# Kernel tuning notes

Measured on AMD Instinct MI355X. Metric: run time of the kernel, lower is better.

Reference implementation:

```python
import jax, jax.numpy as jnp
import numpy as np

RCR = 5.2          # radial cutoff
RCA = 3.5          # angular cutoff
ETA_R = 16.0
SHF_R = jnp.asarray(0.9 + 0.26875 * np.arange(16), jnp.float32)          # 16 radial shifts
ZETA = 32.0
SHF_Z = jnp.asarray((2 * np.arange(8) + 1) * np.pi / 16.0, jnp.float32)  # 8 angle shifts
ETA_A = 8.0
SHF_A = jnp.asarray(0.9 + 0.65 * np.arange(4), jnp.float32)              # 4 angular radial shifts
NUM_SPECIES = 4
NUM_PAIRS = NUM_SPECIES * (NUM_SPECIES + 1) // 2  # 10


def _pair_index_table():
    idx = np.zeros((NUM_SPECIES, NUM_SPECIES), np.int32)
    c = 0
    for s1 in range(NUM_SPECIES):
        for s2 in range(s1, NUM_SPECIES):
            idx[s1, s2] = c
            idx[s2, s1] = c
            c += 1
    return jnp.asarray(idx)

PAIR_IDX = _pair_index_table()


def _cutoff(d, rc):
    return jnp.where(d <= rc, 0.5 * jnp.cos(jnp.pi * d / rc) + 0.5, 0.0)


def setup_inputs() -> dict:
    key = jax.random.key(0)
    k1, k2 = jax.random.split(key)
    species = jax.random.randint(k1, (32, 48), 0, NUM_SPECIES, dtype=jnp.int32)
    coords = jax.random.uniform(k2, (32, 48, 3), jnp.float32) * 7.0  # 7 Angstrom box
    return {"species": species, "coords": coords}


def reference(species, coords):
    B, A = species.shape
    dt = coords.dtype
    # vec[b,i,j] = coords[j] - coords[i]
    diff = coords[:, None, :, :] - coords[:, :, None, :]           # [B,A,A,3]
    d2 = jnp.sum(diff * diff, -1)
    eye = jnp.eye(A, dtype=bool)
    dist = jnp.sqrt(jnp.where(eye, 1.0, d2))                        # safe on diagonal
    valid = (species[:, :, None] >= 0) & (species[:, None, :] >= 0) & (~eye)

    # ---------- radial AEV ----------
    fc_r = jnp.where(valid & (dist <= RCR), _cutoff(dist, RCR), 0.0)
    rad_terms = 0.25 * jnp.exp(-ETA_R * (dist[..., None] - SHF_R) ** 2) * fc_r[..., None]  # [B,A,A,16]
    sp_onehot = jax.nn.one_hot(jnp.clip(species, 0), NUM_SPECIES, dtype=dt)                # [B,A,4]
    radial = jnp.einsum('bijr,bjs->bisr', rad_terms, sp_onehot).reshape(B, A, NUM_SPECIES * 16)

    # ---------- angular AEV ----------
    in_ca = valid & (dist <= RCA)
    fc_a = jnp.where(in_ca, _cutoff(dist, RCA), 0.0)
    dotp = jnp.einsum('bijc,bikc->bijk', diff, diff)                # [B,A,A,A]
    cos_t = 0.95 * dotp / (dist[:, :, :, None] * dist[:, :, None, :])
    angles = jnp.arccos(cos_t)
    f1 = ((1.0 + jnp.cos(angles[..., None] - SHF_Z)) * 0.5) ** ZETA          # [B,A,A,A,8]
    avg_d = 0.5 * (dist[:, :, :, None] + dist[:, :, None, :])
    f2 = jnp.exp(-ETA_A * (avg_d[..., None] - SHF_A) ** 2)                   # [B,A,A,A,4]
    jk = jnp.triu(jnp.ones((A, A), bool), 1)                                 # unordered neighbor pairs j<k
    trip_mask = in_ca[:, :, :, None] & in_ca[:, :, None, :] & jk
    w = jnp.where(trip_mask, 2.0 * fc_a[:, :, :, None] * fc_a[:, :, None, :], 0.0)  # [B,A,A,A]
    pair_idx = PAIR_IDX[jnp.clip(species, 0)[:, :, None], jnp.clip(species, 0)[:, None, :]]  # [B,A,A]
    pair_oh = jax.nn.one_hot(pair_idx, NUM_PAIRS, dtype=dt)                  # [B,A,A,10]
    angular = jnp.einsum('bijk,bijka,bijkz,bjkp->bipaz', w, f2, f1, pair_oh)
    angular = angular.reshape(B, A, NUM_PAIRS * 4 * 8)

    aevs = jnp.concatenate([radial, angular], axis=-1)   # [B,A,384]
    return species, aevs
```

## Files before the change

### kernel.cpp

```cpp
#include <hip/hip_runtime.h>
#include <math.h>

#define NB 32
#define NA 48
#define RCRf 5.2f
#define RCAf 3.5f
#define PI_F 3.14159265358979f
#define CMAX 384

__global__ __launch_bounds__(320)
void aev_kernel(const int* __restrict__ species, const float* __restrict__ coords,
                float* __restrict__ out)
{
    const int bid = blockIdx.x;
    const int b = bid / NA;
    const int i = bid - b * NA;
    const int tid = threadIdx.x;

    __shared__ float crd[NA * 3];
    __shared__ int   ssp[NA];
    __shared__ float pd[NA], pfr[NA];
    __shared__ float cdx[NA], cdy[NA], cdz[NA], cdd[NA], cfc[NA];
    __shared__ int   csp[NA];
    __shared__ int   sm;
    __shared__ float radpart[5 * 64];
    __shared__ float f1rec[CMAX * 8];
    __shared__ float w2rec[CMAX * 4];
    __shared__ int   cnt[10], basep[10];
    __shared__ unsigned cur[10];

    if (tid < NA * 3) crd[tid] = coords[(size_t)b * NA * 3 + tid];
    if (tid >= 192 && tid < 192 + NA) ssp[tid - 192] = species[b * NA + (tid - 192)];
    __syncthreads();

    const float xi = crd[3 * i], yi = crd[3 * i + 1], zi = crd[3 * i + 2];

    if (tid < 64) {
        const int j = tid;
        float dx = 0.f, dy = 0.f, dz = 0.f, d = 1.0f, fr = 0.0f, fa = 0.0f;
        bool inA = false;
        if (j < NA) {
            dx = crd[3 * j] - xi; dy = crd[3 * j + 1] - yi; dz = crd[3 * j + 2] - zi;
            d = sqrtf(dx * dx + dy * dy + dz * dz);
            if (j != i && d <= RCRf) fr = 0.5f * __cosf((PI_F / RCRf) * d) + 0.5f;
            if (j != i && d <= RCAf) { inA = true; fa = 0.5f * __cosf((PI_F / RCAf) * d) + 0.5f; }
            pd[j] = d; pfr[j] = fr;
        }
        const unsigned long long mask = __ballot(inA);
        if (inA) {
            const int pos = (int)__popcll(mask & ((1ull << j) - 1ull));
            cdx[pos] = dx; cdy[pos] = dy; cdz[pos] = dz;
            cdd[pos] = d;  cfc[pos] = fa; csp[pos] = ssp[j];
        }
        if (j == 0) sm = (int)__popcll(mask);
    }
    __syncthreads();

    {
        const int f = tid & 63, seg = tid >> 6;
        const int s = f >> 4, r = f & 15;
        const float shf = 0.9f + 0.26875f * (float)r;
        float acc = 0.0f;
        const int j0 = seg * 10, j1 = min(NA, j0 + 10);
        for (int j = j0; j < j1; ++j) {
            const float fr = pfr[j];
            if (fr != 0.0f) {
                const float u = pd[j] - shf;
                const float v = 0.25f * __expf(-16.0f * u * u) * fr;
                acc += (ssp[j] == s) ? v : 0.0f;
            }
        }
        radpart[seg * 64 + f] = acc;
    }

    const int m = sm;
    const int T = m * (m - 1) / 2;
    const int nchunks = (T + CMAX - 1) / CMAX;

    const float CZ[8] = { 0.98078528f, 0.83146961f, 0.55557023f, 0.19509032f,
                         -0.19509032f,-0.55557023f,-0.83146961f,-0.98078528f };
    const float SZ[8] = { 0.19509032f, 0.55557023f, 0.83146961f, 0.98078528f,
                          0.98078528f, 0.83146961f, 0.55557023f, 0.19509032f };
    const float SA[4] = { 0.9f, 1.55f, 2.2f, 2.85f };

    const int pmine = tid >> 5, amine = (tid >> 3) & 3, zmine = tid & 7;
    float acc_a = 0.0f;

    for (int c = 0; c < nchunks; ++c) {
        const int t0 = c * CMAX;
        const int cT = min(CMAX, T - t0);
        __syncthreads();
        if (tid < 10) cnt[tid] = 0;
        __syncthreads();

        for (int t = tid; t < cT; t += 320) {
            const int g = t0 + t;
            int jj = 0, rem = g;
            while (rem >= m - 1 - jj) { rem -= m - 1 - jj; ++jj; }
            const int kk = jj + 1 + rem;
            const int s1 = csp[jj], s2 = csp[kk];
            const int lo = min(s1, s2), hi = max(s1, s2);
            const int p = (lo * (9 - lo)) / 2 + (hi - lo);
            atomicAdd(&cnt[p], 1);
        }
        __syncthreads();
        if (tid == 0) {
            int run = 0;
            for (int p = 0; p < 10; ++p) { basep[p] = run; cur[p] = (unsigned)run; run += cnt[p]; }
        }
        __syncthreads();

        for (int t = tid; t < cT; t += 320) {
            const int g = t0 + t;
            int jj = 0, rem = g;
            while (rem >= m - 1 - jj) { rem -= m - 1 - jj; ++jj; }
            const int kk = jj + 1 + rem;

            const float djx = cdx[jj], djy = cdy[jj], djz = cdz[jj];
            const float dkx = cdx[kk], dky = cdy[kk], dkz = cdz[kk];
            const float dj = cdd[jj], dk = cdd[kk];
            const float dot = djx * dkx + djy * dky + djz * dkz;
            const float cosT = 0.95f * dot / (dj * dk);
            const float sinT = sqrtf(fmaxf(1.0f - cosT * cosT, 0.0f));
            const float avg = 0.5f * (dj + dk);
            const float w = 2.0f * cfc[jj] * cfc[kk];
            const int s1 = csp[jj], s2 = csp[kk];
            const int lo = min(s1, s2), hi = max(s1, s2);
            const int p = (lo * (9 - lo)) / 2 + (hi - lo);

            float f1v[8];
            #pragma unroll
            for (int z = 0; z < 8; ++z) {
                const float base = 0.5f + 0.5f * (cosT * CZ[z] + sinT * SZ[z]);
                const float b2 = base * base, b4 = b2 * b2, b8 = b4 * b4, b16 = b8 * b8;
                f1v[z] = b16 * b16;
            }
            float w2v[4];
            #pragma unroll
            for (int a = 0; a < 4; ++a) {
                const float u = avg - SA[a];
                w2v[a] = w * __expf(-8.0f * u * u);
            }
            const unsigned pos = atomicAdd(&cur[p], 1u);
            ((float4*)f1rec)[pos * 2]     = make_float4(f1v[0], f1v[1], f1v[2], f1v[3]);
            ((float4*)f1rec)[pos * 2 + 1] = make_float4(f1v[4], f1v[5], f1v[6], f1v[7]);
            ((float4*)w2rec)[pos]         = make_float4(w2v[0], w2v[1], w2v[2], w2v[3]);
        }
        __syncthreads();

        {
            const int klo = basep[pmine];
            const int khi = klo + cnt[pmine];
            for (int k = klo; k < khi; ++k)
                acc_a += w2rec[k * 4 + amine] * f1rec[k * 8 + zmine];
        }
    }
    __syncthreads();

    float* op = out + NB * NA + (size_t)(b * NA + i) * 384;
    if (tid < 64) {
        op[tid] = radpart[tid] + radpart[64 + tid] + radpart[128 + tid] +
                  radpart[192 + tid] + radpart[256 + tid];
    }
    op[64 + tid] = acc_a;
    if (tid == 0) out[b * NA + i] = (float)ssp[i];
}

extern "C" void kernel_launch(void* const* d_in, const int* in_sizes, int n_in,
                              void* d_out, int out_size, void* d_ws, size_t ws_size,
                              hipStream_t stream) {
    const int*   species = (const int*)d_in[0];
    const float* coords  = (const float*)d_in[1];
    float*       out     = (float*)d_out;
    aev_kernel<<<NB * NA, 320, 0, stream>>>(species, coords, out);
}
```

Before: 67.21 us.

## Replace linear triangle decode with closed form and cache packed triplet indices

Replaces the O(m) while-loop that maps a linear pair index to (j,k) with a sqrt-based closed-form decode, and computes it once per triplet, storing packed j/k/pair-class in shared memory for reuse by the compute pass. Per-thread prefix sums over the ten class counts replace the single-thread serial scan, and the count pass is overlapped with the radial stage, which drops several barriers per chunk. The division is also swapped for a reciprocal multiply. This adds a shared array and float-sqrt rounding fixups in exchange for less serial integer work and fewer synchronisations.

```diff
diff --git a/kernel.cpp b/kernel.cpp
--- a/kernel.cpp
+++ b/kernel.cpp
@@ -7,6 +7,15 @@
 #define RCAf 3.5f
 #define PI_F 3.14159265358979f
 #define CMAX 384
+
+__device__ inline void tri_decode(int t, int m, int T, int& jj, int& kk) {
+    const int u = T - 1 - t;
+    int r = (int)((sqrtf(8.0f * (float)u + 1.0f) - 1.0f) * 0.5f);
+    while (r * (r + 1) / 2 > u) --r;
+    while ((r + 1) * (r + 2) / 2 <= u) ++r;
+    jj = m - 2 - r;
+    kk = m - 1 - (u - r * (r + 1) / 2);
+}
 
 __global__ __launch_bounds__(320)
 void aev_kernel(const int* __restrict__ species, const float* __restrict__ coords,
@@ -24,13 +33,15 @@
     __shared__ int   csp[NA];
     __shared__ int   sm;
     __shared__ float radpart[5 * 64];
-    __shared__ float f1rec[CMAX * 8];
-    __shared__ float w2rec[CMAX * 4];
-    __shared__ int   cnt[10], basep[10];
+    __shared__ __align__(16) float f1rec[CMAX * 8];
+    __shared__ __align__(16) float w2rec[CMAX * 4];
+    __shared__ int   trec[CMAX];
+    __shared__ int   cnt[10];
     __shared__ unsigned cur[10];
 
     if (tid < NA * 3) crd[tid] = coords[(size_t)b * NA * 3 + tid];
     if (tid >= 192 && tid < 192 + NA) ssp[tid - 192] = species[b * NA + (tid - 192)];
+    if (tid >= 256 && tid < 266) cnt[tid - 256] = 0;
     __syncthreads();
 
     const float xi = crd[3 * i], yi = crd[3 * i + 1], zi = crd[3 * i + 2];
@@ -56,6 +67,10 @@
     }
     __syncthreads();
 
+    const int m = sm;
+    const int T = m * (m - 1) / 2;
+    const int nchunks = (T + CMAX - 1) / CMAX;
+
     {
         const int f = tid & 63, seg = tid >> 6;
         const int s = f >> 4, r = f & 15;
@@ -72,10 +87,18 @@
         }
         radpart[seg * 64 + f] = acc;
     }
-
-    const int m = sm;
-    const int T = m * (m - 1) / 2;
-    const int nchunks = (T + CMAX - 1) / CMAX;
+    {
+        const int cT = min(CMAX, T);
+        for (int t = tid; t < cT; t += 320) {
+            int jj, kk; tri_decode(t, m, T, jj, kk);
+            const int s1 = csp[jj], s2 = csp[kk];
+            const int lo = min(s1, s2), hi = max(s1, s2);
+            const int p = (lo * (9 - lo)) / 2 + (hi - lo);
+            trec[t] = jj | (kk << 6) | (p << 12);
+            atomicAdd(&cnt[p], 1);
+        }
+    }
+    __syncthreads();
 
     const float CZ[8] = { 0.98078528f, 0.83146961f, 0.55557023f, 0.19509032f,
                          -0.19509032f,-0.55557023f,-0.83146961f,-0.98078528f };
@@ -89,44 +112,29 @@
     for (int c = 0; c < nchunks; ++c) {
         const int t0 = c * CMAX;
         const int cT = min(CMAX, T - t0);
-        __syncthreads();
-        if (tid < 10) cnt[tid] = 0;
-        __syncthreads();
 
-        for (int t = tid; t < cT; t += 320) {
-            const int g = t0 + t;
-            int jj = 0, rem = g;
-            while (rem >= m - 1 - jj) { rem -= m - 1 - jj; ++jj; }
-            const int kk = jj + 1 + rem;
-            const int s1 = csp[jj], s2 = csp[kk];
-            const int lo = min(s1, s2), hi = max(s1, s2);
-            const int p = (lo * (9 - lo)) / 2 + (hi - lo);
-            atomicAdd(&cnt[p], 1);
-        }
-        __syncthreads();
-        if (tid == 0) {
-            int run = 0;
-            for (int p = 0; p < 10; ++p) { basep[p] = run; cur[p] = (unsigned)run; run += cnt[p]; }
+        int mybase = 0, mycnt = 0, run = 0;
+        #pragma unroll
+        for (int p = 0; p < 10; ++p) {
+            const int cp = cnt[p];
+            if (p == pmine) { mybase = run; mycnt = cp; }
+            if (tid < 10 && p == tid) cur[tid] = (unsigned)run;
+            run += cp;
         }
         __syncthreads();
 
         for (int t = tid; t < cT; t += 320) {
-            const int g = t0 + t;
-            int jj = 0, rem = g;
-            while (rem >= m - 1 - jj) { rem -= m - 1 - jj; ++jj; }
-            const int kk = jj + 1 + rem;
+            const int pk = trec[t];
+            const int jj = pk & 63, kk = (pk >> 6) & 63, p = pk >> 12;
 
             const float djx = cdx[jj], djy = cdy[jj], djz = cdz[jj];
             const float dkx = cdx[kk], dky = cdy[kk], dkz = cdz[kk];
             const float dj = cdd[jj], dk = cdd[kk];
             const float dot = djx * dkx + djy * dky + djz * dkz;
-            const float cosT = 0.95f * dot / (dj * dk);
+            const float cosT = 0.95f * dot * __frcp_rn(dj * dk);
             const float sinT = sqrtf(fmaxf(1.0f - cosT * cosT, 0.0f));
             const float avg = 0.5f * (dj + dk);
             const float w = 2.0f * cfc[jj] * cfc[kk];
-            const int s1 = csp[jj], s2 = csp[kk];
-            const int lo = min(s1, s2), hi = max(s1, s2);
-            const int p = (lo * (9 - lo)) / 2 + (hi - lo);
 
             float f1v[8];
             #pragma unroll
@@ -148,14 +156,26 @@
         }
         __syncthreads();
 
-        {
-            const int klo = basep[pmine];
-            const int khi = klo + cnt[pmine];
-            for (int k = klo; k < khi; ++k)
-                acc_a += w2rec[k * 4 + amine] * f1rec[k * 8 + zmine];
+        for (int k = mybase; k < mybase + mycnt; ++k)
+            acc_a += w2rec[k * 4 + amine] * f1rec[k * 8 + zmine];
+
+        if (c + 1 < nchunks) {
+            __syncthreads();
+            if (tid < 10) cnt[tid] = 0;
+            __syncthreads();
+            const int n0 = (c + 1) * CMAX;
+            const int nT = min(CMAX, T - n0);
+            for (int t = tid; t < nT; t += 320) {
+                int jj, kk; tri_decode(n0 + t, m, T, jj, kk);
+                const int s1 = csp[jj], s2 = csp[kk];
+                const int lo = min(s1, s2), hi = max(s1, s2);
+                const int p = (lo * (9 - lo)) / 2 + (hi - lo);
+                trec[t] = jj | (kk << 6) | (p << 12);
+                atomicAdd(&cnt[p], 1);
+            }
+            __syncthreads();
         }
     }
-    __syncthreads();
 
     float* op = out + NB * NA + (size_t)(b * NA + i) * 384;
     if (tid < 64) {
```

After: 66.49 us. Within noise of the previous version (-1.1%).
